# Kernel optimization log

Hardware: AMD Instinct MI355X
Metric: run time of the kernel (lower is better)

## Reference

```python
import jax, jax.numpy as jnp
import numpy as np

EPS_LN = 1e-5
EPS_SM = 1e-16  # PyG softmax denominator epsilon


def setup_inputs() -> dict:
    key = jax.random.key(0)
    k1, k2, k3 = jax.random.split(key, 3)
    N = 100000          # total nodes
    Q, C = 4, 128       # num_querys, hidden_channels
    M = Q * C           # multi_hidden_channels = 512
    B = 512             # batch_size (num graphs)
    x = jax.random.normal(k1, (N, M), dtype=jnp.float32)
    W_nlin = jax.random.normal(k2, (M, M), dtype=jnp.float32) * 0.02
    b_nlin = jnp.zeros((M,), dtype=jnp.float32)
    querys = jnp.ones((Q, C), dtype=jnp.float32)  # q_scale = 1.0 fill
    graph_idx = jnp.sort(jax.random.randint(k3, (N,), 0, B, dtype=jnp.int32))
    return {"x": x, "W_nlin": W_nlin, "b_nlin": b_nlin, "querys": querys,
            "graph_idx": graph_idx, "batch_size": B}


def reference(x, W_nlin, b_nlin, querys, graph_idx, batch_size):
    Q, C = querys.shape
    # nlin: MLP(1 layer, multi_hidden_channels, act=True) -> Linear + ReLU
    h = jax.nn.relu(x @ W_nlin + b_nlin)          # [N, Q*C]
    h = h.reshape(-1, Q, C)                       # [N, Q, C]
    # LayerNorm over hidden_channels, no affine
    mu = jnp.mean(h, axis=-1, keepdims=True)
    var = jnp.mean(jnp.square(h - mu), axis=-1, keepdims=True)
    q = (h - mu) * jax.lax.rsqrt(var + EPS_LN) * querys[None]  # [N, Q, C]
    # segment softmax over nodes within each graph (elementwise in Q, C)
    seg_max = jax.ops.segment_max(q, graph_idx, num_segments=batch_size)  # [B, Q, C]
    e = jnp.exp(q - seg_max[graph_idx])
    seg_sum = jax.ops.segment_sum(e, graph_idx, num_segments=batch_size)
    a = e / (seg_sum[graph_idx] + EPS_SM)         # [N, Q, C]
    # weighted scatter-sum pooling per graph
    r = jax.ops.segment_sum(a * h, graph_idx, num_segments=batch_size)   # [B, Q, C]
    # out_method='lin' with n_agg_trans=0 -> agglin is identity
    return r.reshape(batch_size, -1)              # [B, Q*C]
```

## Files before the change

### kernel.cpp

```cpp
#include <hip/hip_runtime.h>
#include <hip/hip_bf16.h>
#include <stdint.h>

typedef __attribute__((ext_vector_type(8))) short bf16x8;
typedef __attribute__((ext_vector_type(4))) float f32x4;
typedef __attribute__((ext_vector_type(8))) unsigned short ushort8;

__device__ __forceinline__ unsigned short cvt1(float f) {
  union { __hip_bfloat16 b; unsigned short u; } v;
  v.b = __float2bfloat16(f);
  return v.u;
}

__device__ __forceinline__ void gld_lds16(const void* g, void* l) {
  __builtin_amdgcn_global_load_lds(
      (const __attribute__((address_space(1))) unsigned int*)g,
      (__attribute__((address_space(3))) unsigned int*)l,
      16, 0, 0);
}

#define SM_OFS 12.0f

__global__ void cast_wt_kernel(const float* __restrict__ W,
                               unsigned short* __restrict__ wt) {
  int t = blockIdx.x * blockDim.x + threadIdx.x;
  int n = t >> 9;
  int k = t & 511;
  wt[t] = cvt1(W[k * 512 + n]);
}

__global__ __launch_bounds__(256, 4) void gemm_fused_kernel(
    const float* __restrict__ x,
    const unsigned short* __restrict__ wt,
    const float* __restrict__ bias,
    const float* __restrict__ qs,
    const int* __restrict__ gidx,
    float* __restrict__ NU,
    float* __restrict__ SA,
    int N, int mtiles) {
  __shared__ __align__(16) char smem[16384 + 8192];
  char* AsB = smem;
  char* BsB = smem + 16384;

  const int nfull = (mtiles >> 3) << 3;
  const int full_bids = nfull * 4;
  int mtile, ntile;
  {
    const int bid = blockIdx.x;
    if (bid < full_bids) {
      const int chunk = bid >> 5, j = bid & 31;
      mtile = (chunk << 3) + (j & 7);
      ntile = j >> 3;
    } else {
      const int j = bid - full_bids;
      const int rem = mtiles - nfull;
      mtile = nfull + j % rem;
      ntile = j / rem;
    }
  }
  const int m0 = mtile << 7;
  const int n0 = ntile << 7;

  const int tid = threadIdx.x;
  const int lane = tid & 63;
  const int wid = tid >> 6;
  const int wr = wid >> 1;
  const int wc = wid & 1;

  f32x4 acc[4][4];
#pragma unroll
  for (int m = 0; m < 4; m++)
#pragma unroll
    for (int n = 0; n < 4; n++) acc[m][n] = (f32x4){0.f, 0.f, 0.f, 0.f};

  const float* aP[4];
  int aLds[4];
#pragma unroll
  for (int L = 0; L < 4; L++) {
    const int p = (L << 12) + tid * 16;
    const int row = p >> 7;
    const int slot = (p >> 4) & 7;
    const int k4 = slot ^ (row & 7);
    aP[L] = x + (long)min(m0 + row, N - 1) * 512 + k4 * 4;
    aLds[L] = (L << 12) + (wid << 10);
  }

  const unsigned short* bP[2];
  int bLds[2];
#pragma unroll
  for (int L = 0; L < 2; L++) {
    const int p = (L << 12) + tid * 16;
    const int row = p >> 6;
    const int slot = (p >> 4) & 3;
    const int k8 = slot ^ ((row >> 1) & 3);
    bP[L] = wt + (long)(n0 + row) * 512 + k8 * 8;
    bLds[L] = (L << 12) + (wid << 10);
  }

  const int rsel = lane & 15;
  const int k8l = lane >> 4;
  int offA[4], offB[4];
#pragma unroll
  for (int m = 0; m < 4; m++) {
    const int ra = wr * 64 + m * 16 + rsel;
    offA[m] = ra * 128 + (((k8l << 1) ^ (ra & 7)) << 4);
    const int rb = wc * 64 + m * 16 + rsel;
    offB[m] = rb * 64 + ((k8l ^ ((rb >> 1) & 3)) << 4);
  }

#pragma unroll
  for (int t = 0; t < 16; t++) {
#pragma unroll
    for (int L = 0; L < 4; L++) gld_lds16(aP[L] + (t << 5), AsB + aLds[L]);
#pragma unroll
    for (int L = 0; L < 2; L++) gld_lds16(bP[L] + (t << 5), BsB + bLds[L]);
    __syncthreads();

    bf16x8 af[4], bq[4];
#pragma unroll
    for (int m = 0; m < 4; m++) {
      const f32x4 r0 = *(const f32x4*)(AsB + offA[m]);
      const f32x4 r1 = *(const f32x4*)(AsB + (offA[m] ^ 16));
      ushort8 u;
      u[0] = cvt1(r0[0]); u[1] = cvt1(r0[1]);
      u[2] = cvt1(r0[2]); u[3] = cvt1(r0[3]);
      u[4] = cvt1(r1[0]); u[5] = cvt1(r1[1]);
      u[6] = cvt1(r1[2]); u[7] = cvt1(r1[3]);
      af[m] = (bf16x8)u;
    }
#pragma unroll
    for (int n = 0; n < 4; n++) bq[n] = *(const bf16x8*)(BsB + offB[n]);
#pragma unroll
    for (int m = 0; m < 4; m++)
#pragma unroll
      for (int n = 0; n < 4; n++)
        acc[m][n] = __builtin_amdgcn_mfma_f32_16x16x32_bf16(
            af[m], bq[n], acc[m][n], 0, 0, 0);
    __syncthreads();
  }

  int* sgidx = (int*)smem;
  float* sS = (float*)(smem + 512);
  float* sQ = (float*)(smem + 1536);

  if (tid < 128) {
    const long rg = (long)m0 + tid;
    sgidx[tid] = (rg < N) ? gidx[rg] : 0x7fffffff;
  }

  const int colb = n0 + wc * 64 + rsel;
  float bval[4], qsv[4];
#pragma unroll
  for (int n = 0; n < 4; n++) {
    bval[n] = bias[colb + n * 16];
    qsv[n] = qs[colb + n * 16];
  }

#pragma unroll
  for (int m = 0; m < 4; m++) {
#pragma unroll
    for (int i = 0; i < 4; i++) {
      const int row_l = wr * 64 + m * 16 + (k8l << 2) + i;
      float s = 0.f, q = 0.f;
#pragma unroll
      for (int n = 0; n < 4; n++) {
        float v = fmaxf(acc[m][n][i] + bval[n], 0.f);
        s += v;
        q += v * v;
      }
#pragma unroll
      for (int d = 1; d < 16; d <<= 1) {
        s += __shfl_xor(s, d, 64);
        q += __shfl_xor(q, d, 64);
      }
      if (rsel == 0) {
        sS[row_l * 2 + wc] = s;
        sQ[row_l * 2 + wc] = q;
      }
    }
  }
  __syncthreads();

  const int lastv = min(127, (int)((long)N - 1 - (long)m0));
  if (wr * 64 <= lastv) {
    const int gmin = sgidx[wr * 64];
    const int gmax = sgidx[min(wr * 64 + 63, lastv)];
    for (int g = gmin; g <= gmax; ++g) {
      float num[4] = {0.f, 0.f, 0.f, 0.f};
      float den[4] = {0.f, 0.f, 0.f, 0.f};
#pragma unroll
      for (int m = 0; m < 4; m++) {
#pragma unroll
        for (int i = 0; i < 4; i++) {
          const int row_l = wr * 64 + m * 16 + (k8l << 2) + i;
          if (sgidx[row_l] == g) {
            const float s = sS[row_l * 2] + sS[row_l * 2 + 1];
            const float qq = sQ[row_l * 2] + sQ[row_l * 2 + 1];
            const float mean = s * (1.f / 128.f);
            const float var = qq * (1.f / 128.f) - mean * mean;
            const float rstd = rsqrtf(var + 1e-5f);
#pragma unroll
            for (int n = 0; n < 4; n++) {
              const float v = fmaxf(acc[m][n][i] + bval[n], 0.f);
              const float qv = (v - mean) * rstd * qsv[n];
              const float e = __expf(qv - SM_OFS);
              num[n] += e * v;
              den[n] += e;
            }
          }
        }
      }
#pragma unroll
      for (int n = 0; n < 4; n++) {
        num[n] += __shfl_xor(num[n], 16, 64);
        num[n] += __shfl_xor(num[n], 32, 64);
        den[n] += __shfl_xor(den[n], 16, 64);
        den[n] += __shfl_xor(den[n], 32, 64);
      }
      if (k8l == 0) {
#pragma unroll
        for (int n = 0; n < 4; n++) {
          atomicAdd(&NU[(long)g * 512 + colb + n * 16], num[n]);
          atomicAdd(&SA[(long)g * 512 + colb + n * 16], den[n]);
        }
      }
    }
  }
}

__global__ void finalize_kernel(const float* __restrict__ NU,
                                const float* __restrict__ SA,
                                float* __restrict__ out, int total) {
  const int i = blockIdx.x * blockDim.x + threadIdx.x;
  if (i < total) out[i] = NU[i] / (SA[i] + 1e-16f);
}

extern "C" void kernel_launch(void* const* d_in, const int* in_sizes, int n_in,
                              void* d_out, int out_size, void* d_ws, size_t ws_size,
                              hipStream_t stream) {
  const float* x = (const float*)d_in[0];
  const float* W = (const float*)d_in[1];
  const float* bias = (const float*)d_in[2];
  const float* qs = (const float*)d_in[3];
  const int* gidx = (const int*)d_in[4];
  const int N = in_sizes[0] / 512;
  const int B = out_size / 512;
  float* out = (float*)d_out;

  char* ws = (char*)d_ws;
  size_t off = 0;
  auto alloc = [&](size_t bytes) {
    char* p = ws + off;
    off += (bytes + 255) & ~(size_t)255;
    return p;
  };
  unsigned short* wt = (unsigned short*)alloc((size_t)512 * 512 * 2);
  float* accbuf = (float*)alloc((size_t)B * 512 * 2 * sizeof(float));
  float* NU = accbuf;
  float* SA = accbuf + (size_t)B * 512;
  (void)ws_size;

  hipMemsetAsync(accbuf, 0, (size_t)B * 512 * 2 * sizeof(float), stream);
  cast_wt_kernel<<<(512 * 512) / 256, 256, 0, stream>>>(W, wt);
  const int mtiles = (N + 127) / 128;
  gemm_fused_kernel<<<mtiles * 4, 256, 0, stream>>>(x, wt, bias, qs, gidx, NU,
                                                    SA, N, mtiles);
  const int total = B * 512;
  finalize_kernel<<<(total + 255) / 256, 256, 0, stream>>>(NU, SA, out, total);
}
```

Measured before the change: 130.8 us.

## Double-buffer LDS tiles to overlap global loads with MFMA compute

Doubles the shared memory to two stages and prefetches the next K-tile with global_load_lds while the current tile is converted and fed to MFMAs. The two barriers per iteration become one wait plus barrier. Launch bounds drop from 4 to 3 blocks per CU to fit the larger LDS footprint, trading occupancy for overlap of memory latency within a block. There is a possible hazard: the prefetch writes the buffer that other waves may still have been reading in the previous iteration, but the barrier at the end of each iteration guards it.

```diff
diff --git a/kernel.cpp b/kernel.cpp
--- a/kernel.cpp
+++ b/kernel.cpp
@@ -29,7 +29,7 @@
   wt[t] = cvt1(W[k * 512 + n]);
 }
 
-__global__ __launch_bounds__(256, 4) void gemm_fused_kernel(
+__global__ __launch_bounds__(256, 3) void gemm_fused_kernel(
     const float* __restrict__ x,
     const unsigned short* __restrict__ wt,
     const float* __restrict__ bias,
@@ -38,9 +38,7 @@
     float* __restrict__ NU,
     float* __restrict__ SA,
     int N, int mtiles) {
-  __shared__ __align__(16) char smem[16384 + 8192];
-  char* AsB = smem;
-  char* BsB = smem + 16384;
+  __shared__ __align__(16) char smem[2 * 24576];
 
   const int nfull = (mtiles >> 3) << 3;
   const int full_bids = nfull * 4;
@@ -108,14 +106,26 @@
     offB[m] = rb * 64 + ((k8l ^ ((rb >> 1) & 3)) << 4);
   }
 
+#define STAGE(buf, tt)                                                     \
+  {                                                                        \
+    _Pragma("unroll") for (int L = 0; L < 4; L++)                          \
+        gld_lds16(aP[L] + ((tt) << 5), smem + (buf) * 24576 + aLds[L]);    \
+    _Pragma("unroll") for (int L = 0; L < 2; L++)                          \
+        gld_lds16(bP[L] + ((tt) << 5),                                     \
+                  smem + (buf) * 24576 + 16384 + bLds[L]);                 \
+  }
+
+  STAGE(0, 0);
+  asm volatile("s_waitcnt vmcnt(0)" ::: "memory");
+  __builtin_amdgcn_sched_barrier(0);
+  __builtin_amdgcn_s_barrier();
+
 #pragma unroll
   for (int t = 0; t < 16; t++) {
-#pragma unroll
-    for (int L = 0; L < 4; L++) gld_lds16(aP[L] + (t << 5), AsB + aLds[L]);
-#pragma unroll
-    for (int L = 0; L < 2; L++) gld_lds16(bP[L] + (t << 5), BsB + bLds[L]);
-    __syncthreads();
-
+    if (t < 15) STAGE((t + 1) & 1, t + 1);
+
+    const char* AsB = smem + (t & 1) * 24576;
+    const char* BsB = AsB + 16384;
     bf16x8 af[4], bq[4];
 #pragma unroll
     for (int m = 0; m < 4; m++) {
@@ -136,9 +146,16 @@
       for (int n = 0; n < 4; n++)
         acc[m][n] = __builtin_amdgcn_mfma_f32_16x16x32_bf16(
             af[m], bq[n], acc[m][n], 0, 0, 0);
-    __syncthreads();
-  }
-
+
+    if (t < 15) {
+      asm volatile("s_waitcnt vmcnt(0)" ::: "memory");
+      __builtin_amdgcn_sched_barrier(0);
+      __builtin_amdgcn_s_barrier();
+    }
+  }
+#undef STAGE
+
+  __syncthreads();
   int* sgidx = (int*)smem;
   float* sS = (float*)(smem + 512);
   float* sQ = (float*)(smem + 1536);
```

New measurement: 127.1 us. 2.8% less time.

## Double-buffer GEMM mainloop and convert A to bf16 once before LDS

Applied to the files above, without the earlier changes.

Replaces the single-buffered direct-to-LDS fp32 A staging with register prefetch of the next K-slice, a one-time bf16 conversion per element, and a write into a second LDS buffer. B loads are also double-buffered, so the loop needs one barrier per iteration instead of two and global loads overlap the MFMA work. A tiles now take half the LDS space and the redundant per-wave fp32-to-bf16 conversions go away. In exchange the kernel uses more registers (occupancy hint lowered from 4 to 3) and more LDS in total.

```diff
diff --git a/kernel.cpp b/kernel.cpp
--- a/kernel.cpp
+++ b/kernel.cpp
@@ -29,7 +29,7 @@
   wt[t] = cvt1(W[k * 512 + n]);
 }
 
-__global__ __launch_bounds__(256, 4) void gemm_fused_kernel(
+__global__ __launch_bounds__(256, 3) void gemm_fused_kernel(
     const float* __restrict__ x,
     const unsigned short* __restrict__ wt,
     const float* __restrict__ bias,
@@ -38,9 +38,7 @@
     float* __restrict__ NU,
     float* __restrict__ SA,
     int N, int mtiles) {
-  __shared__ __align__(16) char smem[16384 + 8192];
-  char* AsB = smem;
-  char* BsB = smem + 16384;
+  __shared__ __align__(16) char smem[2 * 16384];
 
   const int nfull = (mtiles >> 3) << 3;
   const int full_bids = nfull * 4;
@@ -73,17 +71,12 @@
 #pragma unroll
     for (int n = 0; n < 4; n++) acc[m][n] = (f32x4){0.f, 0.f, 0.f, 0.f};
 
-  const float* aP[4];
-  int aLds[4];
-#pragma unroll
-  for (int L = 0; L < 4; L++) {
-    const int p = (L << 12) + tid * 16;
-    const int row = p >> 7;
-    const int slot = (p >> 4) & 7;
-    const int k4 = slot ^ (row & 7);
-    aP[L] = x + (long)min(m0 + row, N - 1) * 512 + k4 * 4;
-    aLds[L] = (L << 12) + (wid << 10);
-  }
+  const int arow = tid >> 1;
+  const int akh = tid & 1;
+  const float* aSrc = x + (long)min(m0 + arow, N - 1) * 512 + akh * 16;
+  const int aswz = (arow >> 1) & 3;
+  const int aDst0 = arow * 64 + ((((akh << 1) | 0) ^ aswz) << 4);
+  const int aDst1 = arow * 64 + ((((akh << 1) | 1) ^ aswz) << 4);
 
   const unsigned short* bP[2];
   int bLds[2];
@@ -103,31 +96,61 @@
 #pragma unroll
   for (int m = 0; m < 4; m++) {
     const int ra = wr * 64 + m * 16 + rsel;
-    offA[m] = ra * 128 + (((k8l << 1) ^ (ra & 7)) << 4);
+    offA[m] = ra * 64 + ((k8l ^ ((ra >> 1) & 3)) << 4);
     const int rb = wc * 64 + m * 16 + rsel;
     offB[m] = rb * 64 + ((k8l ^ ((rb >> 1) & 3)) << 4);
   }
 
+  float4 av[4];
+
+#define LOAD_A(tt)                                          \
+  {                                                         \
+    const float4* ap = (const float4*)(aSrc + ((tt) << 5)); \
+    av[0] = ap[0];                                          \
+    av[1] = ap[1];                                          \
+    av[2] = ap[2];                                          \
+    av[3] = ap[3];                                          \
+  }
+
+#define WRITE_A(buf)                                        \
+  {                                                         \
+    ushort8 o0, o1;                                         \
+    o0[0] = cvt1(av[0].x); o0[1] = cvt1(av[0].y);           \
+    o0[2] = cvt1(av[0].z); o0[3] = cvt1(av[0].w);           \
+    o0[4] = cvt1(av[1].x); o0[5] = cvt1(av[1].y);           \
+    o0[6] = cvt1(av[1].z); o0[7] = cvt1(av[1].w);           \
+    o1[0] = cvt1(av[2].x); o1[1] = cvt1(av[2].y);           \
+    o1[2] = cvt1(av[2].z); o1[3] = cvt1(av[2].w);           \
+    o1[4] = cvt1(av[3].x); o1[5] = cvt1(av[3].y);           \
+    o1[6] = cvt1(av[3].z); o1[7] = cvt1(av[3].w);           \
+    *(ushort8*)(smem + (buf) * 16384 + aDst0) = o0;         \
+    *(ushort8*)(smem + (buf) * 16384 + aDst1) = o1;         \
+  }
+
+#define STAGE_B(buf, tt)                                                   \
+  {                                                                        \
+    _Pragma("unroll") for (int L = 0; L < 2; L++)                          \
+        gld_lds16(bP[L] + ((tt) << 5),                                     \
+                  smem + (buf) * 16384 + 8192 + bLds[L]);                  \
+  }
+
+  LOAD_A(0);
+  STAGE_B(0, 0);
+  WRITE_A(0);
+  __syncthreads();
+
 #pragma unroll
   for (int t = 0; t < 16; t++) {
-#pragma unroll
-    for (int L = 0; L < 4; L++) gld_lds16(aP[L] + (t << 5), AsB + aLds[L]);
-#pragma unroll
-    for (int L = 0; L < 2; L++) gld_lds16(bP[L] + (t << 5), BsB + bLds[L]);
-    __syncthreads();
-
+    if (t < 15) {
+      LOAD_A(t + 1);
+      STAGE_B((t + 1) & 1, t + 1);
+    }
+
+    const char* AsB = smem + (t & 1) * 16384;
+    const char* BsB = AsB + 8192;
     bf16x8 af[4], bq[4];
 #pragma unroll
-    for (int m = 0; m < 4; m++) {
-      const f32x4 r0 = *(const f32x4*)(AsB + offA[m]);
-      const f32x4 r1 = *(const f32x4*)(AsB + (offA[m] ^ 16));
-      ushort8 u;
-      u[0] = cvt1(r0[0]); u[1] = cvt1(r0[1]);
-      u[2] = cvt1(r0[2]); u[3] = cvt1(r0[3]);
-      u[4] = cvt1(r1[0]); u[5] = cvt1(r1[1]);
-      u[6] = cvt1(r1[2]); u[7] = cvt1(r1[3]);
-      af[m] = (bf16x8)u;
-    }
+    for (int m = 0; m < 4; m++) af[m] = *(const bf16x8*)(AsB + offA[m]);
 #pragma unroll
     for (int n = 0; n < 4; n++) bq[n] = *(const bf16x8*)(BsB + offB[n]);
 #pragma unroll
@@ -136,9 +159,17 @@
       for (int n = 0; n < 4; n++)
         acc[m][n] = __builtin_amdgcn_mfma_f32_16x16x32_bf16(
             af[m], bq[n], acc[m][n], 0, 0, 0);
-    __syncthreads();
-  }
-
+
+    if (t < 15) {
+      WRITE_A((t + 1) & 1);
+      __syncthreads();
+    }
+  }
+#undef LOAD_A
+#undef WRITE_A
+#undef STAGE_B
+
+  __syncthreads();
   int* sgidx = (int*)smem;
   float* sS = (float*)(smem + 512);
   float* sQ = (float*)(smem + 1536);
```

New measurement: 136.2 us. 1.04x slower.
